# Kernel tuning notes

Hardware: AMD Instinct MI355X
Metric: run time of the kernel (lower is better)

## Reference

```python
import jax, jax.numpy as jnp
import numpy as np

B, H, S, D = 4, 16, 2048, 64

def setup_inputs() -> dict:
    key = jax.random.key(0)
    kq, kk, kv, km = jax.random.split(key, 4)
    q = jax.random.normal(kq, (B, H, S, D), dtype=jnp.float32)
    k = jax.random.normal(kk, (B, H, S, D), dtype=jnp.float32)
    v = jax.random.normal(kv, (B, H, S, D), dtype=jnp.float32)
    scale = jnp.float32(1.0 / np.sqrt(D))
    attn_mask = jax.random.bernoulli(km, 0.5, (B, H, S, S))  # True = masked
    return {"q": q, "k": k, "v": v, "scale": scale, "attn_mask": attn_mask}

def reference(q, k, v, scale, attn_mask):
    # scores: [B, H, S, S]
    scores = jnp.einsum('bhqd,bhkd->bhqk', q, k) * scale
    # faithful to torch masked_fill_(attn_mask, 1e-09): masked positions set to 1e-9 (NOT -inf)
    scores = jnp.where(attn_mask, jnp.float32(1e-9), scores)
    attention = jax.nn.softmax(scores, axis=-1)
    # dropout is identity in eval mode (deterministic reference)
    context = jnp.einsum('bhqk,bhkd->bhqd', attention, v)
    return (context, attention)
```

## Files before the change

kernel.cpp:

```cpp
#include <hip/hip_runtime.h>
#include <stdint.h>

#define B_ 4
#define H_ 16
#define S_ 2048
#define D_ 64
#define NWIN 64
#define EBS 40
#define VBS 40

typedef __attribute__((ext_vector_type(8))) short short8;
typedef __attribute__((ext_vector_type(4))) float float4v;
typedef __attribute__((ext_vector_type(4))) unsigned int uint4v;
typedef __attribute__((ext_vector_type(2))) unsigned int uint2v;

static __device__ __forceinline__ short f2bf(float f) {
  uint32_t u = __builtin_bit_cast(uint32_t, f);
  u = (u + 0x7FFFu + ((u >> 16) & 1u)) >> 16;
  return (short)u;
}
static __device__ __forceinline__ float bf2f(uint32_t s) {
  return __builtin_bit_cast(float, s << 16);
}
static __device__ __forceinline__ uint32_t cvtpk(float lo, float hi) {
  uint32_t r;
  asm("v_cvt_pk_bf16_f32 %0, %1, %2" : "=v"(r) : "v"(lo), "v"(hi));
  return r;
}
static __device__ __forceinline__ uint32_t nz4(uint32_t d) {
  uint32_t x = (d & 0x7F7F7F7Fu) + 0x7F7F7F7Fu;
  x = (x | d) & 0x80808080u;
  return x >> 7;
}
static __device__ __forceinline__ uint32_t nib(uint32_t d) {
  return ((nz4(d) * 0x01020408u) >> 24) & 0xFu;
}

#define LINV_OFF   ((size_t)64)
#define LINV_BYTES ((size_t)B_ * H_ * S_ * 4)
#define KBF_OFF    (LINV_OFF + LINV_BYTES)
#define KBF_BYTES  ((size_t)B_ * H_ * S_ * D_ * 2)
#define VT_OFF     (KBF_OFF + KBF_BYTES)
#define VT_BYTES   ((size_t)B_ * H_ * S_ * D_ * 2)
#define MB_OFF     (VT_OFF + VT_BYTES)
#define MB_BYTES   ((size_t)B_ * H_ * S_ * 64 * 4)

__global__ void detect_mask_dtype(const uint8_t* __restrict__ m, uint32_t* flag) {
  uint32_t a = 0, b = 0;
  for (int i = threadIdx.x; i < 65536; i += 256) {
    uint8_t x = m[i];
    if (i & 3) a |= x; else b |= x;
  }
  uint32_t bits = (a ? 1u : 0u) | (b ? 2u : 0u);
  if (bits) atomicOr(flag, bits);
}

__global__ __launch_bounds__(256) void prep_k(const float* __restrict__ K,
                                              short* __restrict__ Kbf) {
  size_t base = ((size_t)blockIdx.x * 256 + threadIdx.x) * 8;
  float4v a = *(const float4v*)(K + base);
  float4v b = *(const float4v*)(K + base + 4);
  short8 o;
  o[0]=f2bf(a.x); o[1]=f2bf(a.y); o[2]=f2bf(a.z); o[3]=f2bf(a.w);
  o[4]=f2bf(b.x); o[5]=f2bf(b.y); o[6]=f2bf(b.z); o[7]=f2bf(b.w);
  *(short8*)(Kbf + base) = o;
}

__global__ __launch_bounds__(256) void prep_vt(const float* __restrict__ V,
                                               short* __restrict__ VT) {
  __shared__ short tile[64][72];
  int bh = blockIdx.x >> 5, k0 = (blockIdx.x & 31) * 64;
  const float* src = V + ((size_t)bh * S_ + k0) * D_;
  int t = threadIdx.x;
  int r = t >> 2, c0 = (t & 3) * 16;
#pragma unroll
  for (int j = 0; j < 4; ++j) {
    float4v f = *(const float4v*)(src + (size_t)r * D_ + c0 + j * 4);
    tile[r][c0 + j*4 + 0] = f2bf(f.x);
    tile[r][c0 + j*4 + 1] = f2bf(f.y);
    tile[r][c0 + j*4 + 2] = f2bf(f.z);
    tile[r][c0 + j*4 + 3] = f2bf(f.w);
  }
  __syncthreads();
  int d = t >> 2, ks0 = (t & 3) * 16;
  short* dst = VT + (size_t)bh * D_ * S_ + (size_t)d * S_ + k0 + ks0;
#pragma unroll
  for (int half = 0; half < 2; ++half) {
    short8 o;
#pragma unroll
    for (int i = 0; i < 8; ++i) o[i] = tile[ks0 + half * 8 + i][d];
    *(short8*)(dst + half * 8) = o;
  }
}

template <int PREP, int BM>
__global__ __launch_bounds__(512, 6) void k_sums(
    const float* __restrict__ Q, const float* __restrict__ K,
    const float* __restrict__ V, const float* __restrict__ scale_p,
    const uint8_t* __restrict__ M, const uint32_t* __restrict__ flag,
    const short* __restrict__ Kbf, const short* __restrict__ VT,
    float* __restrict__ linvG, uint32_t* __restrict__ mbitsG,
    float* __restrict__ outC)
{
  __shared__ uint32_t mbits[128 * 66];
  __shared__ short kbuf[2][32 * 64];
  __shared__ short vbuf[2][64 * VBS];
  __shared__ short ebounce[8][16 * EBS];

  const int bx  = (blockIdx.x & 7) * 128 + (blockIdx.x >> 3);
  const int bh  = bx >> 4;
  const int q0  = (bx & 15) * 128;

  const int tid  = threadIdx.x;
  const int widx = tid >> 6;
  const int lane = tid & 63;
  const int g    = lane >> 4;
  const int c    = lane & 15;
  const int qrow = q0 + widx * 16 + c;

  const float scale = scale_p[0];
  const uint32_t fl = flag[0];

  const short* Kbp = Kbf + (size_t)bh * S_ * D_;
  const short* VTp = VT + (size_t)bh * D_ * S_;
  const float* Kfp = K + (size_t)bh * S_ * D_;
  const float* Vfp = V + (size_t)bh * S_ * D_;

  {
    const int row = tid >> 2;
    const int wq0 = (tid & 3) * 16;
    if (fl == 3u) {
      const uint8_t* mrow = M + ((size_t)(bh * S_ + q0 + row)) * S_ + wq0 * 32;
#pragma unroll
      for (int j = 0; j < 16; ++j) {
        uint4v a = *(const uint4v*)(mrow + j * 32);
        uint4v b = *(const uint4v*)(mrow + j * 32 + 16);
        mbits[row * 65 + wq0 + j] =
            nib(a.x) | (nib(a.y) << 4) | (nib(a.z) << 8)  | (nib(a.w) << 12)
          | (nib(b.x) << 16) | (nib(b.y) << 20) | (nib(b.z) << 24) | (nib(b.w) << 28);
      }
    } else {
      const uint32_t* mrow = (const uint32_t*)M + ((size_t)(bh * S_ + q0 + row)) * S_ + wq0 * 32;
#pragma unroll
      for (int j = 0; j < 16; ++j) {
        uint32_t bits = 0;
#pragma unroll
        for (int u = 0; u < 8; ++u) {
          uint4v wv = *(const uint4v*)(mrow + j * 32 + u * 4);
          uint32_t nzb = (wv.x ? 1u : 0u) | (wv.y ? 2u : 0u) | (wv.z ? 4u : 0u) | (wv.w ? 8u : 0u);
          bits |= nzb << (u * 4);
        }
        mbits[row * 65 + wq0 + j] = bits;
      }
    }
  }

  short8 qB[2];
  {
    const float* qr = Q + ((size_t)(bh * S_ + qrow)) * D_;
    float4v x0 = *(const float4v*)(qr + g * 8);
    float4v x1 = *(const float4v*)(qr + g * 8 + 4);
    float4v y0 = *(const float4v*)(qr + 32 + g * 8);
    float4v y1 = *(const float4v*)(qr + 32 + g * 8 + 4);
    short8 f;
    f[0]=f2bf(x0.x); f[1]=f2bf(x0.y); f[2]=f2bf(x0.z); f[3]=f2bf(x0.w);
    f[4]=f2bf(x1.x); f[5]=f2bf(x1.y); f[6]=f2bf(x1.z); f[7]=f2bf(x1.w);
    qB[0] = f;
    f[0]=f2bf(y0.x); f[1]=f2bf(y0.y); f[2]=f2bf(y0.z); f[3]=f2bf(y0.w);
    f[4]=f2bf(y1.x); f[5]=f2bf(y1.y); f[6]=f2bf(y1.z); f[7]=f2bf(y1.w);
    qB[1] = f;
  }

  const bool kstager = (widx < 4);
  const bool vstager = (widx >= 4) && (PREP != 0);
  const int  sr = (widx << 3) + (lane >> 3);
  const int  sp = lane & 7;
  const int  sdst = sr * 64 + ((sp ^ (sr & 7)) << 3);
  const int  vr = ((widx - 4) << 4) + (lane >> 2);
  const int  vp = lane & 3;
  short8  kreg, vreg;
  float4v kf0, kf1;
#define ISSUE(W) do {                                                          \
    if (kstager) {                                                             \
      if (PREP) kreg = *(const short8*)(Kbp + (size_t)((W) * 32 + sr) * 64 + sp * 8); \
      else { const float* s_ = Kfp + (size_t)((W) * 32 + sr) * 64 + sp * 8;    \
             kf0 = *(const float4v*)s_; kf1 = *(const float4v*)(s_ + 4); }     \
    } else if (vstager) {                                                      \
      vreg = *(const short8*)(VTp + (size_t)vr * S_ + (W) * 32 + vp * 8);      \
    } } while (0)
#define WRITE(BUF) do {                                                        \
    if (kstager) {                                                             \
      short8 o_;                                                               \
      if (PREP) o_ = kreg;                                                     \
      else { o_[0]=f2bf(kf0.x); o_[1]=f2bf(kf0.y); o_[2]=f2bf(kf0.z); o_[3]=f2bf(kf0.w); \
             o_[4]=f2bf(kf1.x); o_[5]=f2bf(kf1.y); o_[6]=f2bf(kf1.z); o_[7]=f2bf(kf1.w); } \
      *(short8*)&kbuf[BUF][sdst] = o_;                                         \
    } else if (vstager) {                                                      \
      *(short8*)&vbuf[BUF][vr * VBS + vp * 8] = vreg;                          \
    } } while (0)

  const int ka0 = ((g       ^ (c & 7)) << 3);
  const int ka1 = (((g + 4) ^ (c & 7)) << 3);
  const uint32_t* mrow = &mbits[(widx * 16 + c) * 65];

  ISSUE(0); WRITE(0); ISSUE(1);
  __syncthreads();

  if (BM) {
    uint32_t* mg = mbitsG + ((size_t)(bh * S_ + q0)) * 64;
#pragma unroll
    for (int i = 0; i < 16; ++i) {
      const int wdx = i * 512 + tid;
      const int row = wdx >> 6, wir = wdx & 63;
      __builtin_nontemporal_store(mbits[row * 65 + wir], mg + wdx);
    }
  }

  float rsv = 0.0f;
  float4v cacc[4];
#pragma unroll
  for (int nd = 0; nd < 4; ++nd) cacc[nd] = (float4v){0.f, 0.f, 0.f, 0.f};
  short* eb = &ebounce[widx][0];

#pragma unroll 1
  for (int w = 0; w < NWIN; ++w) {
    const int cur = w & 1;
    const int kwin = w * 32;

    short8 vA0, vA1, vA2, vA3;
    if (PREP) {
      const short* vb = &vbuf[cur][0];
      vA0 = *(const short8*)(vb + (size_t)(c)      * VBS + g * 8);
      vA1 = *(const short8*)(vb + (size_t)(16 + c) * VBS + g * 8);
      vA2 = *(const short8*)(vb + (size_t)(32 + c) * VBS + g * 8);
      vA3 = *(const short8*)(vb + (size_t)(48 + c) * VBS + g * 8);
    } else {
      const float* vc = Vfp + (size_t)(kwin + g * 8) * D_ + c;
#pragma unroll
      for (int e = 0; e < 8; ++e) {
        vA0[e] = f2bf(vc[(size_t)e * D_]);
        vA1[e] = f2bf(vc[(size_t)e * D_ + 16]);
        vA2[e] = f2bf(vc[(size_t)e * D_ + 32]);
        vA3[e] = f2bf(vc[(size_t)e * D_ + 48]);
      }
    }

    const short* kb = &kbuf[cur][0];
    short8 a0 = *(const short8*)(kb + c * 64 + ka0);
    short8 a1 = *(const short8*)(kb + c * 64 + ka1);
    short8 a2 = *(const short8*)(kb + (c + 16) * 64 + ka0);
    short8 a3 = *(const short8*)(kb + (c + 16) * 64 + ka1);

    float4v acc0 = (float4v){0.f,0.f,0.f,0.f};
    float4v acc1 = (float4v){0.f,0.f,0.f,0.f};
    acc0 = __builtin_amdgcn_mfma_f32_16x16x32_bf16(a0, qB[0], acc0, 0, 0, 0);
    acc0 = __builtin_amdgcn_mfma_f32_16x16x32_bf16(a1, qB[1], acc0, 0, 0, 0);
    acc1 = __builtin_amdgcn_mfma_f32_16x16x32_bf16(a2, qB[0], acc1, 0, 0, 0);
    acc1 = __builtin_amdgcn_mfma_f32_16x16x32_bf16(a3, qB[1], acc1, 0, 0, 0);

    const uint32_t mw = mrow[w];
    float e0[4], e1[4];
#pragma unroll
    for (int r = 0; r < 4; ++r) {
      e0[r] = ((mw >> (4 * g + r)) & 1u)      ? 1.0f : __expf(acc0[r] * scale);
      e1[r] = ((mw >> (16 + 4 * g + r)) & 1u) ? 1.0f : __expf(acc1[r] * scale);
      rsv += e0[r] + e1[r];
    }
    uint2v lo, hi2;
    lo.x  = cvtpk(e0[0], e0[1]);  lo.y  = cvtpk(e0[2], e0[3]);
    hi2.x = cvtpk(e1[0], e1[1]);  hi2.y = cvtpk(e1[2], e1[3]);
    *(uint2v*)&eb[c * EBS + 4 * g]      = lo;
    *(uint2v*)&eb[c * EBS + 16 + 4 * g] = hi2;
    const short8 bfrag = *(const short8*)&eb[c * EBS + g * 8];

    cacc[0] = __builtin_amdgcn_mfma_f32_16x16x32_bf16(vA0, bfrag, cacc[0], 0, 0, 0);
    cacc[1] = __builtin_amdgcn_mfma_f32_16x16x32_bf16(vA1, bfrag, cacc[1], 0, 0, 0);
    cacc[2] = __builtin_amdgcn_mfma_f32_16x16x32_bf16(vA2, bfrag, cacc[2], 0, 0, 0);
    cacc[3] = __builtin_amdgcn_mfma_f32_16x16x32_bf16(vA3, bfrag, cacc[3], 0, 0, 0);

    if (w + 1 < NWIN) {
      WRITE(cur ^ 1);
      if (w + 2 < NWIN) ISSUE(w + 2);
      __syncthreads();
    }
  }
#undef ISSUE
#undef WRITE

  rsv += __shfl_xor(rsv, 16);
  rsv += __shfl_xor(rsv, 32);
  const float linv = 1.0f / rsv;
  if (g == 0) linvG[(size_t)bh * S_ + qrow] = linv;
  __syncthreads();

  {
    float* cst = (float*)mbits;
#pragma unroll
    for (int nd = 0; nd < 4; ++nd) {
      float4v v;
#pragma unroll
      for (int r = 0; r < 4; ++r) v[r] = cacc[nd][r] * linv;
      *(float4v*)&cst[(widx * 16 + c) * 66 + nd * 16 + 4 * g] = v;
    }
    __syncthreads();
    const int qq = tid >> 2, ch = tid & 3;
    const float* src = &cst[qq * 66 + ch * 16];
    float* dst = outC + ((size_t)(bh * S_ + q0 + qq)) * D_ + ch * 16;
    float4v c0 = *(const float4v*)src;
    float4v c1 = *(const float4v*)(src + 4);
    float4v c2 = *(const float4v*)(src + 8);
    float4v c3 = *(const float4v*)(src + 12);
    __builtin_nontemporal_store(c0, (float4v*)dst);
    __builtin_nontemporal_store(c1, (float4v*)(dst + 4));
    __builtin_nontemporal_store(c2, (float4v*)(dst + 8));
    __builtin_nontemporal_store(c3, (float4v*)(dst + 12));
  }
}

template <int PREP, int BM>
__global__ __launch_bounds__(256, 7) void k_store(
    const float* __restrict__ Q, const float* __restrict__ K,
    const float* __restrict__ scale_p, const uint8_t* __restrict__ M,
    const uint32_t* __restrict__ flag, const short* __restrict__ Kbf,
    const float* __restrict__ linvG, const uint32_t* __restrict__ mbitsG,
    float* __restrict__ outA)
{
  __shared__ uint32_t mbits2[64 * 68];
  __shared__ short eb2[4][16 * EBS];

  const int bx  = (blockIdx.x & 7) * 256 + (blockIdx.x >> 3);
  const int bh  = bx >> 5;
  const int q0  = (bx & 31) * 64;

  const int tid  = threadIdx.x;
  const int wv   = tid >> 6;
  const int lane = tid & 63;
  const int g    = lane >> 4;
  const int c    = lane & 15;
  const int qrow = q0 + wv * 16 + c;

  const float scale = scale_p[0];
  const uint32_t fl = flag[0];

  const short* Kbp = Kbf + (size_t)bh * S_ * D_;
  const float* Kfp = K + (size_t)bh * S_ * D_;

  if (BM) {
    const uint32_t* mg = mbitsG + ((size_t)(bh * S_ + q0)) * 64;
#pragma unroll
    for (int i = 0; i < 4; ++i) {
      const int idx4 = i * 256 + tid;
      uint4v v = *(const uint4v*)(mg + (size_t)idx4 * 4);
      const int w0 = idx4 * 4, row = w0 >> 6, wir = w0 & 63;
      *(uint4v*)&mbits2[row * 68 + wir] = v;
    }
  } else {
    const int row = tid >> 2;
    const int wq0 = (tid & 3) * 16;
    if (fl == 3u) {
      const uint8_t* mrow = M + ((size_t)(bh * S_ + q0 + row)) * S_ + wq0 * 32;
#pragma unroll
      for (int j = 0; j < 16; ++j) {
        uint4v a = *(const uint4v*)(mrow + j * 32);
        uint4v b = *(const uint4v*)(mrow + j * 32 + 16);
        mbits2[row * 68 + wq0 + j] =
            nib(a.x) | (nib(a.y) << 4) | (nib(a.z) << 8)  | (nib(a.w) << 12)
          | (nib(b.x) << 16) | (nib(b.y) << 20) | (nib(b.z) << 24) | (nib(b.w) << 28);
      }
    } else {
      const uint32_t* mrow = (const uint32_t*)M + ((size_t)(bh * S_ + q0 + row)) * S_ + wq0 * 32;
#pragma unroll
      for (int j = 0; j < 16; ++j) {
        uint32_t bits = 0;
#pragma unroll
        for (int u = 0; u < 8; ++u) {
          uint4v wvv = *(const uint4v*)(mrow + j * 32 + u * 4);
          uint32_t nzb = (wvv.x ? 1u : 0u) | (wvv.y ? 2u : 0u) | (wvv.z ? 4u : 0u) | (wvv.w ? 8u : 0u);
          bits |= nzb << (u * 4);
        }
        mbits2[row * 68 + wq0 + j] = bits;
      }
    }
  }

  short8 qB[2];
  {
    const float* qr = Q + ((size_t)(bh * S_ + qrow)) * D_;
    float4v x0 = *(const float4v*)(qr + g * 8);
    float4v x1 = *(const float4v*)(qr + g * 8 + 4);
    float4v y0 = *(const float4v*)(qr + 32 + g * 8);
    float4v y1 = *(const float4v*)(qr + 32 + g * 8 + 4);
    short8 f;
    f[0]=f2bf(x0.x); f[1]=f2bf(x0.y); f[2]=f2bf(x0.z); f[3]=f2bf(x0.w);
    f[4]=f2bf(x1.x); f[5]=f2bf(x1.y); f[6]=f2bf(x1.z); f[7]=f2bf(x1.w);
    qB[0] = f;
    f[0]=f2bf(y0.x); f[1]=f2bf(y0.y); f[2]=f2bf(y0.z); f[3]=f2bf(y0.w);
    f[4]=f2bf(y1.x); f[5]=f2bf(y1.y); f[6]=f2bf(y1.z); f[7]=f2bf(y1.w);
    qB[1] = f;
  }
  const float linvq = linvG[(size_t)bh * S_ + qrow];
  __syncthreads();

  const uint32_t* mrow = &mbits2[(wv * 16 + c) * 68];
  short* eb = &eb2[wv][0];
  const int srow = lane >> 3;
  const int scol = lane & 7;
  float* arow0 = outA + ((size_t)(bh * S_ + q0 + wv * 16 + srow)) * S_ + scol * 4;
  float* arow1 = outA + ((size_t)(bh * S_ + q0 + wv * 16 + srow + 8)) * S_ + scol * 4;

#pragma unroll 1
  for (int w = 0; w < NWIN; ++w) {
    const int kwin = w * 32;

    float4v acc0 = (float4v){0.f,0.f,0.f,0.f};
    float4v acc1 = (float4v){0.f,0.f,0.f,0.f};
    if (PREP) {
      const short* kr = Kbp + (size_t)(kwin + c) * D_ + g * 8;
      short8 a0 = *(const short8*)kr;
      short8 a1 = *(const short8*)(kr + 32);
      const short* kr1 = kr + 16 * D_;
      short8 a2 = *(const short8*)kr1;
      short8 a3 = *(const short8*)(kr1 + 32);
      acc0 = __builtin_amdgcn_mfma_f32_16x16x32_bf16(a0, qB[0], acc0, 0, 0, 0);
      acc0 = __builtin_amdgcn_mfma_f32_16x16x32_bf16(a1, qB[1], acc0, 0, 0, 0);
      acc1 = __builtin_amdgcn_mfma_f32_16x16x32_bf16(a2, qB[0], acc1, 0, 0, 0);
      acc1 = __builtin_amdgcn_mfma_f32_16x16x32_bf16(a3, qB[1], acc1, 0, 0, 0);
    } else {
      const float* kr = Kfp + (size_t)(kwin + c) * D_ + g * 8;
      const float* kr1 = kr + 16 * D_;
      short8 a0, a1, a2, a3;
#pragma unroll
      for (int e = 0; e < 8; ++e) {
        a0[e] = f2bf(kr[e]);  a1[e] = f2bf(kr[32 + e]);
        a2[e] = f2bf(kr1[e]); a3[e] = f2bf(kr1[32 + e]);
      }
      acc0 = __builtin_amdgcn_mfma_f32_16x16x32_bf16(a0, qB[0], acc0, 0, 0, 0);
      acc0 = __builtin_amdgcn_mfma_f32_16x16x32_bf16(a1, qB[1], acc0, 0, 0, 0);
      acc1 = __builtin_amdgcn_mfma_f32_16x16x32_bf16(a2, qB[0], acc1, 0, 0, 0);
      acc1 = __builtin_amdgcn_mfma_f32_16x16x32_bf16(a3, qB[1], acc1, 0, 0, 0);
    }

    const uint32_t mw = mrow[w];
    float n0[4], n1[4];
#pragma unroll
    for (int r = 0; r < 4; ++r) {
      n0[r] = (((mw >> (4 * g + r)) & 1u)      ? 1.0f : __expf(acc0[r] * scale)) * linvq;
      n1[r] = (((mw >> (16 + 4 * g + r)) & 1u) ? 1.0f : __expf(acc1[r] * scale)) * linvq;
    }
    uint2v lo, hi2;
    lo.x  = cvtpk(n0[0], n0[1]);  lo.y  = cvtpk(n0[2], n0[3]);
    hi2.x = cvtpk(n1[0], n1[1]);  hi2.y = cvtpk(n1[2], n1[3]);
    *(uint2v*)&eb[c * EBS + 4 * g]      = lo;
    *(uint2v*)&eb[c * EBS + 16 + 4 * g] = hi2;

    const uint2v ev0 = *(const uint2v*)&eb[srow * EBS + scol * 4];
    const uint2v ev1 = *(const uint2v*)&eb[(srow + 8) * EBS + scol * 4];
    float4v s0, s1;
    s0.x = bf2f(ev0.x & 0xffff); s0.y = bf2f(ev0.x >> 16);
    s0.z = bf2f(ev0.y & 0xffff); s0.w = bf2f(ev0.y >> 16);
    s1.x = bf2f(ev1.x & 0xffff); s1.y = bf2f(ev1.x >> 16);
    s1.z = bf2f(ev1.y & 0xffff); s1.w = bf2f(ev1.y >> 16);
    __builtin_nontemporal_store(s0, (float4v*)(arow0 + kwin));
    __builtin_nontemporal_store(s1, (float4v*)(arow1 + kwin));
  }
}

extern "C" void kernel_launch(void* const* d_in, const int* in_sizes, int n_in,
                              void* d_out, int out_size, void* d_ws, size_t ws_size,
                              hipStream_t stream) {
  const float*   Q     = (const float*)d_in[0];
  const float*   K     = (const float*)d_in[1];
  const float*   V     = (const float*)d_in[2];
  const float*   scale = (const float*)d_in[3];
  const uint8_t* M     = (const uint8_t*)d_in[4];
  uint32_t* flag  = (uint32_t*)d_ws;
  float*    linvG = (float*)((char*)d_ws + LINV_OFF);
  short*    Kbf   = (short*)((char*)d_ws + KBF_OFF);
  short*    VT    = (short*)((char*)d_ws + VT_OFF);
  uint32_t* mbG   = (uint32_t*)((char*)d_ws + MB_OFF);
  float* outC = (float*)d_out;
  float* outA = outC + (size_t)B_ * H_ * S_ * D_;

  hipMemsetAsync(flag, 0, 4, stream);
  detect_mask_dtype<<<dim3(1), dim3(256), 0, stream>>>(M, flag);

  const bool prep = ws_size >= VT_OFF + VT_BYTES;
  const bool bm   = ws_size >= MB_OFF + MB_BYTES;
  const int grid1 = B_ * H_ * (S_ / 128);
  const int grid2 = B_ * H_ * (S_ / 64);

  if (prep) {
    prep_k<<<dim3((B_ * H_ * S_ * D_) / (256 * 8)), dim3(256), 0, stream>>>(K, Kbf);
    prep_vt<<<dim3(B_ * H_ * (S_ / 64)), dim3(256), 0, stream>>>(V, VT);
    if (bm) {
      k_sums<1, 1><<<dim3(grid1), dim3(512), 0, stream>>>(
          Q, K, V, scale, M, flag, Kbf, VT, linvG, mbG, outC);
      k_store<1, 1><<<dim3(grid2), dim3(256), 0, stream>>>(
          Q, K, scale, M, flag, Kbf, linvG, mbG, outA);
    } else {
      k_sums<1, 0><<<dim3(grid1), dim3(512), 0, stream>>>(
          Q, K, V, scale, M, flag, Kbf, VT, linvG, mbG, outC);
      k_store<1, 0><<<dim3(grid2), dim3(256), 0, stream>>>(
          Q, K, scale, M, flag, Kbf, linvG, mbG, outA);
    }
  } else {
    k_sums<0, 0><<<dim3(grid1), dim3(512), 0, stream>>>(
        Q, K, V, scale, M, flag, Kbf, VT, linvG, mbG, outC);
    k_store<0, 0><<<dim3(grid2), dim3(256), 0, stream>>>(
        Q, K, scale, M, flag, Kbf, linvG, mbG, outA);
  }
}
```

Measured before the change: 823.3 us.

## Stream mask bit-packing in chunks to shrink LDS footprint in k_sums

```diff
diff --git a/kernel.cpp b/kernel.cpp
--- a/kernel.cpp
+++ b/kernel.cpp
@@ -8,6 +8,7 @@
 #define NWIN 64
 #define EBS 40
 #define VBS 40
+#define MSTR 17
 
 typedef __attribute__((ext_vector_type(8))) short short8;
 typedef __attribute__((ext_vector_type(4))) float float4v;
@@ -102,10 +103,11 @@
     float* __restrict__ linvG, uint32_t* __restrict__ mbitsG,
     float* __restrict__ outC)
 {
-  __shared__ uint32_t mbits[128 * 66];
-  __shared__ short kbuf[2][32 * 64];
-  __shared__ short vbuf[2][64 * VBS];
-  __shared__ short ebounce[8][16 * EBS];
+  __shared__ char smemraw[46080];
+  uint32_t* mstrA = (uint32_t*)smemraw;
+  short*    kbufA = (short*)(smemraw + 17408);
+  short*    vbufA = (short*)(smemraw + 25600);
+  short*    ebA   = (short*)(smemraw + 35840);
 
   const int bx  = (blockIdx.x & 7) * 128 + (blockIdx.x >> 3);
   const int bh  = bx >> 4;
@@ -126,34 +128,43 @@
   const float* Kfp = K + (size_t)bh * S_ * D_;
   const float* Vfp = V + (size_t)bh * S_ * D_;
 
-  {
-    const int row = tid >> 2;
-    const int wq0 = (tid & 3) * 16;
-    if (fl == 3u) {
-      const uint8_t* mrow = M + ((size_t)(bh * S_ + q0 + row)) * S_ + wq0 * 32;
-#pragma unroll
-      for (int j = 0; j < 16; ++j) {
-        uint4v a = *(const uint4v*)(mrow + j * 32);
-        uint4v b = *(const uint4v*)(mrow + j * 32 + 16);
-        mbits[row * 65 + wq0 + j] =
-            nib(a.x) | (nib(a.y) << 4) | (nib(a.z) << 8)  | (nib(a.w) << 12)
-          | (nib(b.x) << 16) | (nib(b.y) << 20) | (nib(b.z) << 24) | (nib(b.w) << 28);
-      }
-    } else {
-      const uint32_t* mrow = (const uint32_t*)M + ((size_t)(bh * S_ + q0 + row)) * S_ + wq0 * 32;
-#pragma unroll
-      for (int j = 0; j < 16; ++j) {
-        uint32_t bits = 0;
-#pragma unroll
-        for (int u = 0; u < 8; ++u) {
-          uint4v wv = *(const uint4v*)(mrow + j * 32 + u * 4);
-          uint32_t nzb = (wv.x ? 1u : 0u) | (wv.y ? 2u : 0u) | (wv.z ? 4u : 0u) | (wv.w ? 8u : 0u);
-          bits |= nzb << (u * 4);
-        }
-        mbits[row * 65 + wq0 + j] = bits;
-      }
-    }
-  }
+  const int brow_ = tid >> 2;
+  const int bwb0_ = (tid & 3) * 4;
+#define BUILDHALF(CC, HF) do {                                                 \
+    const int wb_ = bwb0_ + (HF) * 2;                                          \
+    uint32_t w0_, w1_;                                                         \
+    if (fl == 3u) {                                                            \
+      const uint8_t* mp_ = M + ((size_t)(bh * S_ + q0 + brow_)) * S_           \
+                             + (CC) * 512 + wb_ * 32;                          \
+      uint4v a0_ = *(const uint4v*)mp_;                                        \
+      uint4v b0_ = *(const uint4v*)(mp_ + 16);                                 \
+      uint4v a1_ = *(const uint4v*)(mp_ + 32);                                 \
+      uint4v b1_ = *(const uint4v*)(mp_ + 48);                                 \
+      w0_ = nib(a0_.x) | (nib(a0_.y) << 4) | (nib(a0_.z) << 8)  | (nib(a0_.w) << 12) \
+          | (nib(b0_.x) << 16) | (nib(b0_.y) << 20) | (nib(b0_.z) << 24) | (nib(b0_.w) << 28); \
+      w1_ = nib(a1_.x) | (nib(a1_.y) << 4) | (nib(a1_.z) << 8)  | (nib(a1_.w) << 12) \
+          | (nib(b1_.x) << 16) | (nib(b1_.y) << 20) | (nib(b1_.z) << 24) | (nib(b1_.w) << 28); \
+    } else {                                                                   \
+      const uint32_t* mp_ = (const uint32_t*)M                                 \
+          + ((size_t)(bh * S_ + q0 + brow_)) * S_ + (CC) * 512 + wb_ * 32;     \
+      w0_ = 0; w1_ = 0;                                                        \
+      for (int u_ = 0; u_ < 8; ++u_) {                                         \
+        uint4v v_ = *(const uint4v*)(mp_ + u_ * 4);                            \
+        uint32_t nz_ = (v_.x ? 1u : 0u) | (v_.y ? 2u : 0u) | (v_.z ? 4u : 0u) | (v_.w ? 8u : 0u); \
+        w0_ |= nz_ << (u_ * 4);                                                \
+      }                                                                        \
+      for (int u_ = 0; u_ < 8; ++u_) {                                         \
+        uint4v v_ = *(const uint4v*)(mp_ + 32 + u_ * 4);                       \
+        uint32_t nz_ = (v_.x ? 1u : 0u) | (v_.y ? 2u : 0u) | (v_.z ? 4u : 0u) | (v_.w ? 8u : 0u); \
+        w1_ |= nz_ << (u_ * 4);                                                \
+      }                                                                        \
+    }                                                                          \
+    uint32_t* md_ = mstrA + ((CC) & 1) * 128 * MSTR + brow_ * MSTR + wb_;      \
+    md_[0] = w0_; md_[1] = w1_;                                                \
+    if (BM) {                                                                  \
+      uint32_t* mg_ = mbitsG + ((size_t)(bh * 4 + (CC)) * S_ + q0 + brow_) * 16 + wb_; \
+      mg_[0] = w0_; mg_[1] = w1_;                                              \
+    } } while (0)
 
   short8 qB[2];
   {
@@ -194,98 +205,98 @@
       if (PREP) o_ = kreg;                                                     \
       else { o_[0]=f2bf(kf0.x); o_[1]=f2bf(kf0.y); o_[2]=f2bf(kf0.z); o_[3]=f2bf(kf0.w); \
              o_[4]=f2bf(kf1.x); o_[5]=f2bf(kf1.y); o_[6]=f2bf(kf1.z); o_[7]=f2bf(kf1.w); } \
-      *(short8*)&kbuf[BUF][sdst] = o_;                                         \
+      *(short8*)&kbufA[(BUF) * 2048 + sdst] = o_;                              \
     } else if (vstager) {                                                      \
-      *(short8*)&vbuf[BUF][vr * VBS + vp * 8] = vreg;                          \
+      *(short8*)&vbufA[(BUF) * 64 * VBS + vr * VBS + vp * 8] = vreg;           \
     } } while (0)
 
   const int ka0 = ((g       ^ (c & 7)) << 3);
   const int ka1 = (((g + 4) ^ (c & 7)) << 3);
-  const uint32_t* mrow = &mbits[(widx * 16 + c) * 65];
-
+
+  BUILDHALF(0, 0);
+  BUILDHALF(0, 1);
   ISSUE(0); WRITE(0); ISSUE(1);
   __syncthreads();
 
-  if (BM) {
-    uint32_t* mg = mbitsG + ((size_t)(bh * S_ + q0)) * 64;
-#pragma unroll
-    for (int i = 0; i < 16; ++i) {
-      const int wdx = i * 512 + tid;
-      const int row = wdx >> 6, wir = wdx & 63;
-      __builtin_nontemporal_store(mbits[row * 65 + wir], mg + wdx);
-    }
-  }
-
   float rsv = 0.0f;
   float4v cacc[4];
 #pragma unroll
   for (int nd = 0; nd < 4; ++nd) cacc[nd] = (float4v){0.f, 0.f, 0.f, 0.f};
-  short* eb = &ebounce[widx][0];
+  short* eb = ebA + widx * 16 * EBS;
 
 #pragma unroll 1
-  for (int w = 0; w < NWIN; ++w) {
-    const int cur = w & 1;
-    const int kwin = w * 32;
-
-    short8 vA0, vA1, vA2, vA3;
-    if (PREP) {
-      const short* vb = &vbuf[cur][0];
-      vA0 = *(const short8*)(vb + (size_t)(c)      * VBS + g * 8);
-      vA1 = *(const short8*)(vb + (size_t)(16 + c) * VBS + g * 8);
-      vA2 = *(const short8*)(vb + (size_t)(32 + c) * VBS + g * 8);
-      vA3 = *(const short8*)(vb + (size_t)(48 + c) * VBS + g * 8);
-    } else {
-      const float* vc = Vfp + (size_t)(kwin + g * 8) * D_ + c;
-#pragma unroll
-      for (int e = 0; e < 8; ++e) {
-        vA0[e] = f2bf(vc[(size_t)e * D_]);
-        vA1[e] = f2bf(vc[(size_t)e * D_ + 16]);
-        vA2[e] = f2bf(vc[(size_t)e * D_ + 32]);
-        vA3[e] = f2bf(vc[(size_t)e * D_ + 48]);
-      }
-    }
-
-    const short* kb = &kbuf[cur][0];
-    short8 a0 = *(const short8*)(kb + c * 64 + ka0);
-    short8 a1 = *(const short8*)(kb + c * 64 + ka1);
-    short8 a2 = *(const short8*)(kb + (c + 16) * 64 + ka0);
-    short8 a3 = *(const short8*)(kb + (c + 16) * 64 + ka1);
-
-    float4v acc0 = (float4v){0.f,0.f,0.f,0.f};
-    float4v acc1 = (float4v){0.f,0.f,0.f,0.f};
-    acc0 = __builtin_amdgcn_mfma_f32_16x16x32_bf16(a0, qB[0], acc0, 0, 0, 0);
-    acc0 = __builtin_amdgcn_mfma_f32_16x16x32_bf16(a1, qB[1], acc0, 0, 0, 0);
-    acc1 = __builtin_amdgcn_mfma_f32_16x16x32_bf16(a2, qB[0], acc1, 0, 0, 0);
-    acc1 = __builtin_amdgcn_mfma_f32_16x16x32_bf16(a3, qB[1], acc1, 0, 0, 0);
-
-    const uint32_t mw = mrow[w];
-    float e0[4], e1[4];
-#pragma unroll
-    for (int r = 0; r < 4; ++r) {
-      e0[r] = ((mw >> (4 * g + r)) & 1u)      ? 1.0f : __expf(acc0[r] * scale);
-      e1[r] = ((mw >> (16 + 4 * g + r)) & 1u) ? 1.0f : __expf(acc1[r] * scale);
-      rsv += e0[r] + e1[r];
-    }
-    uint2v lo, hi2;
-    lo.x  = cvtpk(e0[0], e0[1]);  lo.y  = cvtpk(e0[2], e0[3]);
-    hi2.x = cvtpk(e1[0], e1[1]);  hi2.y = cvtpk(e1[2], e1[3]);
-    *(uint2v*)&eb[c * EBS + 4 * g]      = lo;
-    *(uint2v*)&eb[c * EBS + 16 + 4 * g] = hi2;
-    const short8 bfrag = *(const short8*)&eb[c * EBS + g * 8];
-
-    cacc[0] = __builtin_amdgcn_mfma_f32_16x16x32_bf16(vA0, bfrag, cacc[0], 0, 0, 0);
-    cacc[1] = __builtin_amdgcn_mfma_f32_16x16x32_bf16(vA1, bfrag, cacc[1], 0, 0, 0);
-    cacc[2] = __builtin_amdgcn_mfma_f32_16x16x32_bf16(vA2, bfrag, cacc[2], 0, 0, 0);
-    cacc[3] = __builtin_amdgcn_mfma_f32_16x16x32_bf16(vA3, bfrag, cacc[3], 0, 0, 0);
-
-    if (w + 1 < NWIN) {
-      WRITE(cur ^ 1);
-      if (w + 2 < NWIN) ISSUE(w + 2);
-      __syncthreads();
+  for (int chunk = 0; chunk < 4; ++chunk) {
+    const uint32_t* mrowc = mstrA + (chunk & 1) * 128 * MSTR + (widx * 16 + c) * MSTR;
+#pragma unroll 1
+    for (int w16 = 0; w16 < 16; ++w16) {
+      const int w = chunk * 16 + w16;
+      const int cur = w & 1;
+      const int kwin = w * 32;
+
+      short8 vA0, vA1, vA2, vA3;
+      if (PREP) {
+        const short* vb = vbufA + cur * 64 * VBS;
+        vA0 = *(const short8*)(vb + (size_t)(c)      * VBS + g * 8);
+        vA1 = *(const short8*)(vb + (size_t)(16 + c) * VBS + g * 8);
+        vA2 = *(const short8*)(vb + (size_t)(32 + c) * VBS + g * 8);
+        vA3 = *(const short8*)(vb + (size_t)(48 + c) * VBS + g * 8);
+      } else {
+        const float* vc = Vfp + (size_t)(kwin + g * 8) * D_ + c;
+#pragma unroll
+        for (int e = 0; e < 8; ++e) {
+          vA0[e] = f2bf(vc[(size_t)e * D_]);
+          vA1[e] = f2bf(vc[(size_t)e * D_ + 16]);
+          vA2[e] = f2bf(vc[(size_t)e * D_ + 32]);
+          vA3[e] = f2bf(vc[(size_t)e * D_ + 48]);
+        }
+      }
+
+      const short* kb = kbufA + cur * 2048;
+      short8 a0 = *(const short8*)(kb + c * 64 + ka0);
+      short8 a1 = *(const short8*)(kb + c * 64 + ka1);
+      short8 a2 = *(const short8*)(kb + (c + 16) * 64 + ka0);
+      short8 a3 = *(const short8*)(kb + (c + 16) * 64 + ka1);
+
+      float4v acc0 = (float4v){0.f,0.f,0.f,0.f};
+      float4v acc1 = (float4v){0.f,0.f,0.f,0.f};
+      acc0 = __builtin_amdgcn_mfma_f32_16x16x32_bf16(a0, qB[0], acc0, 0, 0, 0);
+      acc0 = __builtin_amdgcn_mfma_f32_16x16x32_bf16(a1, qB[1], acc0, 0, 0, 0);
+      acc1 = __builtin_amdgcn_mfma_f32_16x16x32_bf16(a2, qB[0], acc1, 0, 0, 0);
+      acc1 = __builtin_amdgcn_mfma_f32_16x16x32_bf16(a3, qB[1], acc1, 0, 0, 0);
+
+      const uint32_t mw = mrowc[w16];
+      float e0[4], e1[4];
+#pragma unroll
+      for (int r = 0; r < 4; ++r) {
+        e0[r] = ((mw >> (4 * g + r)) & 1u)      ? 1.0f : __expf(acc0[r] * scale);
+        e1[r] = ((mw >> (16 + 4 * g + r)) & 1u) ? 1.0f : __expf(acc1[r] * scale);
+        rsv += e0[r] + e1[r];
+      }
+      uint2v lo, hi2;
+      lo.x  = cvtpk(e0[0], e0[1]);  lo.y  = cvtpk(e0[2], e0[3]);
+      hi2.x = cvtpk(e1[0], e1[1]);  hi2.y = cvtpk(e1[2], e1[3]);
+      *(uint2v*)&eb[c * EBS + 4 * g]      = lo;
+      *(uint2v*)&eb[c * EBS + 16 + 4 * g] = hi2;
+      const short8 bfrag = *(const short8*)&eb[c * EBS + g * 8];
+
+      cacc[0] = __builtin_amdgcn_mfma_f32_16x16x32_bf16(vA0, bfrag, cacc[0], 0, 0, 0);
+      cacc[1] = __builtin_amdgcn_mfma_f32_16x16x32_bf16(vA1, bfrag, cacc[1], 0, 0, 0);
+      cacc[2] = __builtin_amdgcn_mfma_f32_16x16x32_bf16(vA2, bfrag, cacc[2], 0, 0, 0);
+      cacc[3] = __builtin_amdgcn_mfma_f32_16x16x32_bf16(vA3, bfrag, cacc[3], 0, 0, 0);
+
+      if (chunk < 3 && w16 == 4) BUILDHALF(chunk + 1, 0);
+      if (chunk < 3 && w16 == 8) BUILDHALF(chunk + 1, 1);
+
+      if (w + 1 < NWIN) {
+        WRITE(cur ^ 1);
+        if (w + 2 < NWIN) ISSUE(w + 2);
+        __syncthreads();
+      }
     }
   }
 #undef ISSUE
 #undef WRITE
+#undef BUILDHALF
 
   rsv += __shfl_xor(rsv, 16);
   rsv += __shfl_xor(rsv, 32);
@@ -294,26 +305,31 @@
   __syncthreads();
 
   {
-    float* cst = (float*)mbits;
-#pragma unroll
-    for (int nd = 0; nd < 4; ++nd) {
-      float4v v;
-#pragma unroll
-      for (int r = 0; r < 4; ++r) v[r] = cacc[nd][r] * linv;
-      *(float4v*)&cst[(widx * 16 + c) * 66 + nd * 16 + 4 * g] = v;
-    }
-    __syncthreads();
-    const int qq = tid >> 2, ch = tid & 3;
-    const float* src = &cst[qq * 66 + ch * 16];
-    float* dst = outC + ((size_t)(bh * S_ + q0 + qq)) * D_ + ch * 16;
-    float4v c0 = *(const float4v*)src;
-    float4v c1 = *(const float4v*)(src + 4);
-    float4v c2 = *(const float4v*)(src + 8);
-    float4v c3 = *(const float4v*)(src + 12);
-    __builtin_nontemporal_store(c0, (float4v*)dst);
-    __builtin_nontemporal_store(c1, (float4v*)(dst + 4));
-    __builtin_nontemporal_store(c2, (float4v*)(dst + 8));
-    __builtin_nontemporal_store(c3, (float4v*)(dst + 12));
+    float* cst = (float*)smemraw;
+#pragma unroll 1
+    for (int half = 0; half < 2; ++half) {
+      if ((widx >> 2) == half) {
+        const int lr = (widx & 3) * 16 + c;
+#pragma unroll
+        for (int nd = 0; nd < 4; ++nd) {
+          float4v v;
+#pragma unroll
+          for (int r = 0; r < 4; ++r) v[r] = cacc[nd][r] * linv;
+          *(float4v*)&cst[lr * 66 + nd * 16 + 4 * g] = v;
+        }
+      }
+      __syncthreads();
+      {
+        const int qq = tid >> 3, ch = tid & 7;
+        const float* src = &cst[qq * 66 + ch * 8];
+        float* dst = outC + ((size_t)(bh * S_ + q0 + half * 64 + qq)) * D_ + ch * 8;
+        float4v c0 = *(const float4v*)src;
+        float4v c1 = *(const float4v*)(src + 4);
+        __builtin_nontemporal_store(c0, (float4v*)dst);
+        __builtin_nontemporal_store(c1, (float4v*)(dst + 4));
+      }
+      __syncthreads();
+    }
   }
 }
 
@@ -346,13 +362,15 @@
   const float* Kfp = K + (size_t)bh * S_ * D_;
 
   if (BM) {
-    const uint32_t* mg = mbitsG + ((size_t)(bh * S_ + q0)) * 64;
 #pragma unroll
     for (int i = 0; i < 4; ++i) {
-      const int idx4 = i * 256 + tid;
-      uint4v v = *(const uint4v*)(mg + (size_t)idx4 * 4);
-      const int w0 = idx4 * 4, row = w0 >> 6, wir = w0 & 63;
-      *(uint4v*)&mbits2[row * 68 + wir] = v;
+      const int j   = i * 256 + tid;
+      const int cch = j >> 8;
+      const int jj  = j & 255;
+      const int row = jj >> 2, wi4 = (jj & 3) * 4;
+      const uint32_t* mg = mbitsG + ((size_t)(bh * 4 + cch) * S_ + q0 + row) * 16 + wi4;
+      uint4v v = *(const uint4v*)mg;
+      *(uint4v*)&mbits2[row * 68 + cch * 16 + wi4] = v;
     }
   } else {
     const int row = tid >> 2;
```

New measurement: 1.138 ms. 1.38x slower.
